# Performance work log

Measured on AMD Instinct MI355X. Metric: run time of the kernel, lower is better.

The kernel has to match this reference:

```python
import jax, jax.numpy as jnp
import numpy as np
from jax import lax
from jax.scipy.special import logsumexp

B, S, H, L = 64, 512, 1024, 9

def setup_inputs() -> dict:
    key = jax.random.key(0)
    ks = jax.random.split(key, 7)
    return {
        'sequence_output': jax.random.normal(ks[0], (B, S, H), dtype=jnp.float32),
        'tags': jax.random.randint(ks[1], (B, S), 0, L, dtype=jnp.int32),
        'mask': jnp.ones((B, S), dtype=bool),
        'W': jax.random.normal(ks[2], (L, H), dtype=jnp.float32) * 0.02,
        'b': jax.random.normal(ks[3], (L,), dtype=jnp.float32) * 0.02,
        'start_transitions': jax.random.normal(ks[4], (L,), dtype=jnp.float32) * 0.1,
        'end_transitions': jax.random.normal(ks[5], (L,), dtype=jnp.float32) * 0.1,
        'transitions': jax.random.normal(ks[6], (L,), dtype=jnp.float32).repeat(1) if False else jax.random.normal(ks[6], (L, L), dtype=jnp.float32) * 0.1,
    }

def _crf_nll(emissions, tags, mask, start_transitions, end_transitions, transitions):
    # emissions: [B,S,L], tags: [B,S] int, mask: [B,S] bool (mask[:,0] all True)
    Bn, Sn, Ln = emissions.shape
    maskf = mask.astype(emissions.dtype)
    bidx = jnp.arange(Bn)
    # ---- numerator: score of the gold tag sequence ----
    score = start_transitions[tags[:, 0]] + emissions[bidx, 0, tags[:, 0]]
    trans_sc = transitions[tags[:, :-1], tags[:, 1:]]                      # [B,S-1]
    emit_sc = jnp.take_along_axis(emissions, tags[..., None].astype(jnp.int32), axis=2)[..., 0]  # [B,S]
    score = score + jnp.sum((trans_sc + emit_sc[:, 1:]) * maskf[:, 1:], axis=1)
    seq_ends = jnp.sum(mask.astype(jnp.int32), axis=1) - 1                 # [B]
    last_tags = tags[bidx, seq_ends]
    score = score + end_transitions[last_tags]
    # ---- denominator: log partition via forward algorithm (scan over time) ----
    em_t = jnp.swapaxes(emissions, 0, 1)   # [S,B,L]
    mk_t = jnp.swapaxes(mask, 0, 1)        # [S,B]
    alpha0 = start_transitions + em_t[0]   # [B,L]
    def step(alpha, xs):
        em, m = xs
        nxt = logsumexp(alpha[:, :, None] + transitions[None] + em[:, None, :], axis=1)
        alpha = jnp.where(m[:, None], nxt, alpha)
        return alpha, None
    alpha, _ = lax.scan(step, alpha0, (em_t[1:], mk_t[1:]))
    logZ = logsumexp(alpha + end_transitions, axis=1)  # [B]
    llh = jnp.sum(score - logZ)  # reduction='sum'
    return -llh

def reference(sequence_output, tags, mask, W, b, start_transitions, end_transitions, transitions):
    # dropout is identity in eval/reference mode
    emissions = jnp.einsum('bsh,lh->bsl', sequence_output, W) + b
    return _crf_nll(emissions, tags, mask, start_transitions, end_transitions, transitions)
```

## Files before the change

### kernel.cpp

```cpp
#include <hip/hip_runtime.h>
#include <math.h>

#define Bn 64
#define Sn 512
#define Hn 1024
#define Ln 9
#define NC 32
#define KC 16
#define NROWS (Bn * Sn)

__global__ __launch_bounds__(256, 2) void emis_kernel(
    const float* __restrict__ seq, const float* __restrict__ W,
    const float* __restrict__ bias, float* __restrict__ em) {
  const int lane = threadIdx.x & 63;
  const int wave = (int)((blockIdx.x * blockDim.x + threadIdx.x) >> 6);
  const int nwave = (int)((gridDim.x * blockDim.x) >> 6);

  float4 w[Ln][4];
#pragma unroll
  for (int l = 0; l < Ln; ++l)
#pragma unroll
    for (int c = 0; c < 4; ++c)
      w[l][c] = *(const float4*)(W + l * Hn + c * 256 + lane * 4);

  float bl[Ln];
#pragma unroll
  for (int l = 0; l < Ln; ++l) bl[l] = bias[l];

  int row = wave;
  float4 x[4];
  if (row < NROWS) {
    const float* p = seq + (size_t)row * Hn;
#pragma unroll
    for (int c = 0; c < 4; ++c) x[c] = *(const float4*)(p + c * 256 + lane * 4);
  }

  for (; row < NROWS; row += nwave) {
    const int nrow = row + nwave;
    float4 xn[4];
    if (nrow < NROWS) {
      const float* p2 = seq + (size_t)nrow * Hn;
#pragma unroll
      for (int c = 0; c < 4; ++c)
        xn[c] = *(const float4*)(p2 + c * 256 + lane * 4);
    }

    float acc[Ln];
#pragma unroll
    for (int l = 0; l < Ln; ++l) {
      float a = x[0].x * w[l][0].x + x[0].y * w[l][0].y +
                x[0].z * w[l][0].z + x[0].w * w[l][0].w;
#pragma unroll
      for (int c = 1; c < 4; ++c) {
        a += x[c].x * w[l][c].x;
        a += x[c].y * w[l][c].y;
        a += x[c].z * w[l][c].z;
        a += x[c].w * w[l][c].w;
      }
      acc[l] = a;
    }
#pragma unroll
    for (int l = 0; l < Ln; ++l) {
      float v = acc[l];
#pragma unroll
      for (int off = 32; off > 0; off >>= 1) v += __shfl_xor(v, off);
      acc[l] = v;
    }
    if (lane < Ln) {
      float v = acc[0] + bl[0];
#pragma unroll
      for (int l = 1; l < Ln; ++l)
        if (lane == l) v = acc[l] + bl[l];
      em[(size_t)row * Ln + lane] = v;
    }
#pragma unroll
    for (int c = 0; c < 4; ++c) x[c] = xn[c];
  }
}

__global__ __launch_bounds__(128) void crf_chunk_kernel(
    const float* __restrict__ em, const float* __restrict__ trans,
    float* __restrict__ Mout) {
  const int bc = blockIdx.x;
  const int b = bc >> 5, c = bc & (NC - 1);
  const int tid = threadIdx.x;
  __shared__ float Mlds[2][Ln][12];
  __shared__ float emlds[KC * Ln];

  const int t0 = c * KC;
  for (int idx = tid; idx < KC * Ln; idx += 128)
    emlds[idx] = em[((size_t)b * Sn + t0) * Ln + idx];

  const bool act = (tid < 81);
  const int i = tid / 9, j = tid - i * 9;
  float Treg[Ln];
  if (act) {
#pragma unroll
    for (int k = 0; k < Ln; ++k) Treg[k] = trans[k * Ln + j];
  }

  const int tb = (c == 0) ? 1 : t0;
  float val = 0.f;
  if (act) {
    val = trans[i * Ln + j] + emlds[(tb - t0) * Ln + j];
    Mlds[0][i][j] = val;
  }
  __syncthreads();

  int cur = 0;
  for (int t = tb + 1; t < t0 + KC; ++t) {
    if (act) {
      float Mr[Ln];
#pragma unroll
      for (int k = 0; k < Ln; ++k) Mr[k] = Mlds[cur][i][k];
      float e = emlds[(t - t0) * Ln + j];
      float m = Mr[0];
#pragma unroll
      for (int k = 1; k < Ln; ++k) m = fmaxf(m, Mr[k]);
      float s = 0.f;
#pragma unroll
      for (int k = 0; k < Ln; ++k) s += __expf(Mr[k] - m + Treg[k]);
      val = m + __logf(s) + e;
      Mlds[cur ^ 1][i][j] = val;
    }
    __syncthreads();
    cur ^= 1;
  }
  if (act) Mout[(size_t)bc * 81 + tid] = val;
}

__global__ __launch_bounds__(64) void crf_combine_kernel(
    const float* __restrict__ em, const int* __restrict__ tags,
    const float* __restrict__ trans, const float* __restrict__ startT,
    const float* __restrict__ endT, const float* __restrict__ Mall,
    float* __restrict__ out) {
  const int b = blockIdx.x;
  const int lane = threadIdx.x;
  const float* emb = em + (size_t)b * Sn * Ln;
  const int* tg = tags + b * Sn;

  float sc = 0.f;
  for (int t = lane; t < Sn; t += 64) {
    int cur = tg[t];
    if (t == 0) {
      sc += startT[cur] + emb[cur];
    } else {
      int prev = tg[t - 1];
      sc += trans[prev * Ln + cur] + emb[t * Ln + cur];
    }
  }
#pragma unroll
  for (int off = 32; off > 0; off >>= 1) sc += __shfl_xor(sc, off);

  const int j = (lane < Ln) ? lane : 0;
  const float* Mb = Mall + (size_t)b * NC * 81;

  float alpha[Ln];
#pragma unroll
  for (int i = 0; i < Ln; ++i) alpha[i] = startT[i] + emb[i];

  float col[Ln];
#pragma unroll
  for (int i = 0; i < Ln; ++i) col[i] = Mb[i * 9 + j];

  for (int cc = 0; cc < NC; ++cc) {
    float ncol[Ln];
    if (cc + 1 < NC) {
#pragma unroll
      for (int i = 0; i < Ln; ++i) ncol[i] = Mb[(cc + 1) * 81 + i * 9 + j];
    }
    float m = alpha[0];
#pragma unroll
    for (int i = 1; i < Ln; ++i) m = fmaxf(m, alpha[i]);
    float s = 0.f;
#pragma unroll
    for (int i = 0; i < Ln; ++i) s += __expf(alpha[i] - m + col[i]);
    float nxt = m + __logf(s);
#pragma unroll
    for (int i = 0; i < Ln; ++i) alpha[i] = __shfl(nxt, i);
#pragma unroll
    for (int i = 0; i < Ln; ++i) col[i] = ncol[i];
  }

  float mf = alpha[0] + endT[0];
#pragma unroll
  for (int i = 1; i < Ln; ++i) mf = fmaxf(mf, alpha[i] + endT[i]);
  float z = 0.f;
#pragma unroll
  for (int i = 0; i < Ln; ++i) z += __expf(alpha[i] + endT[i] - mf);
  float logZ = mf + __logf(z);

  if (lane == 0) {
    float score = sc + endT[tg[Sn - 1]];
    atomicAdd(out, logZ - score);
  }
}

extern "C" void kernel_launch(void* const* d_in, const int* in_sizes, int n_in,
                              void* d_out, int out_size, void* d_ws, size_t ws_size,
                              hipStream_t stream) {
  const float* seq    = (const float*)d_in[0];
  const int*   tags   = (const int*)d_in[1];
  const float* W      = (const float*)d_in[3];
  const float* bias   = (const float*)d_in[4];
  const float* startT = (const float*)d_in[5];
  const float* endT   = (const float*)d_in[6];
  const float* trans  = (const float*)d_in[7];

  float* em   = (float*)d_ws;
  float* Mall = (float*)((char*)d_ws + (size_t)Bn * Sn * Ln * 4);

  hipMemsetAsync(d_out, 0, sizeof(float), stream);
  emis_kernel<<<1024, 256, 0, stream>>>(seq, W, bias, em);
  crf_chunk_kernel<<<Bn * NC, 128, 0, stream>>>(em, trans, Mall);
  crf_combine_kernel<<<Bn, 64, 0, stream>>>(em, tags, trans, startT, endT, Mall,
                                            (float*)d_out);
}
```

Baseline: 236.7 us.

## Fuse emission GEMV with per-chunk CRF transfer matrices and gold-path scoring

The emission projection and the chunked forward-algorithm kernel are merged into one kernel. Each block computes the 16 emission rows for its chunk into LDS, then builds the chunk's 9x9 log-space transfer matrix from them, so emissions never round-trip through global memory. The gold-path score is now computed per chunk with an atomic, and chunk 0 runs the alpha recursion directly. The combine kernel only folds the remaining chunks. In exchange, each block reloads W into registers and only 4 waves stream 16 rows each, which may expose more load latency than the old persistent grid-stride loop.

```diff
diff --git a/kernel.cpp b/kernel.cpp
--- a/kernel.cpp
+++ b/kernel.cpp
@@ -7,42 +7,49 @@
 #define Ln 9
 #define NC 32
 #define KC 16
-#define NROWS (Bn * Sn)
-
-__global__ __launch_bounds__(256, 2) void emis_kernel(
-    const float* __restrict__ seq, const float* __restrict__ W,
-    const float* __restrict__ bias, float* __restrict__ em) {
-  const int lane = threadIdx.x & 63;
-  const int wave = (int)((blockIdx.x * blockDim.x + threadIdx.x) >> 6);
-  const int nwave = (int)((gridDim.x * blockDim.x) >> 6);
+
+__global__ __launch_bounds__(256, 2) void crf_fused(
+    const float* __restrict__ seq, const int* __restrict__ tags,
+    const float* __restrict__ W, const float* __restrict__ bias,
+    const float* __restrict__ startT, const float* __restrict__ endT,
+    const float* __restrict__ trans, float* __restrict__ Mall,
+    float* __restrict__ alphaBuf, float* __restrict__ out) {
+  const int bc = blockIdx.x;
+  const int b = bc >> 5, c = bc & (NC - 1);
+  const int tid = threadIdx.x;
+  const int lane = tid & 63;
+  const int wv = tid >> 6;
+
+  __shared__ float em_lds[KC][Ln];
+  __shared__ float Mlds[2][Ln][12];
+
+  const int t0 = c * KC;
 
   float4 w[Ln][4];
 #pragma unroll
   for (int l = 0; l < Ln; ++l)
 #pragma unroll
-    for (int c = 0; c < 4; ++c)
-      w[l][c] = *(const float4*)(W + l * Hn + c * 256 + lane * 4);
+    for (int c4 = 0; c4 < 4; ++c4)
+      w[l][c4] = *(const float4*)(W + l * Hn + c4 * 256 + lane * 4);
 
   float bl[Ln];
 #pragma unroll
   for (int l = 0; l < Ln; ++l) bl[l] = bias[l];
 
-  int row = wave;
+  const float* rowbase = seq + ((size_t)b * Sn + t0 + wv * 4) * Hn;
   float4 x[4];
-  if (row < NROWS) {
-    const float* p = seq + (size_t)row * Hn;
-#pragma unroll
-    for (int c = 0; c < 4; ++c) x[c] = *(const float4*)(p + c * 256 + lane * 4);
-  }
-
-  for (; row < NROWS; row += nwave) {
-    const int nrow = row + nwave;
+#pragma unroll
+  for (int c4 = 0; c4 < 4; ++c4)
+    x[c4] = *(const float4*)(rowbase + c4 * 256 + lane * 4);
+
+#pragma unroll
+  for (int r = 0; r < 4; ++r) {
     float4 xn[4];
-    if (nrow < NROWS) {
-      const float* p2 = seq + (size_t)nrow * Hn;
-#pragma unroll
-      for (int c = 0; c < 4; ++c)
-        xn[c] = *(const float4*)(p2 + c * 256 + lane * 4);
+    if (r < 3) {
+      const float* p2 = rowbase + (size_t)(r + 1) * Hn;
+#pragma unroll
+      for (int c4 = 0; c4 < 4; ++c4)
+        xn[c4] = *(const float4*)(p2 + c4 * 256 + lane * 4);
     }
 
     float acc[Ln];
@@ -51,11 +58,11 @@
       float a = x[0].x * w[l][0].x + x[0].y * w[l][0].y +
                 x[0].z * w[l][0].z + x[0].w * w[l][0].w;
 #pragma unroll
-      for (int c = 1; c < 4; ++c) {
-        a += x[c].x * w[l][c].x;
-        a += x[c].y * w[l][c].y;
-        a += x[c].z * w[l][c].z;
-        a += x[c].w * w[l][c].w;
+      for (int c4 = 1; c4 < 4; ++c4) {
+        a += x[c4].x * w[l][c4].x;
+        a += x[c4].y * w[l][c4].y;
+        a += x[c4].z * w[l][c4].z;
+        a += x[c4].w * w[l][c4].w;
       }
       acc[l] = a;
     }
@@ -71,99 +78,110 @@
 #pragma unroll
       for (int l = 1; l < Ln; ++l)
         if (lane == l) v = acc[l] + bl[l];
-      em[(size_t)row * Ln + lane] = v;
-    }
-#pragma unroll
-    for (int c = 0; c < 4; ++c) x[c] = xn[c];
+      em_lds[wv * 4 + r][lane] = v;
+    }
+#pragma unroll
+    for (int c4 = 0; c4 < 4; ++c4) x[c4] = xn[c4];
+  }
+  __syncthreads();
+
+  if (wv == 0) {
+    float g = 0.f;
+    if (lane < KC) {
+      const int t = t0 + lane;
+      const int cur = tags[b * Sn + t];
+      const float e = em_lds[lane][cur];
+      if (t == 0) {
+        g = startT[cur] + e;
+      } else {
+        const int prev = tags[b * Sn + t - 1];
+        g = trans[prev * Ln + cur] + e;
+      }
+      if (t == Sn - 1) g += endT[cur];
+    }
+#pragma unroll
+    for (int off = 8; off > 0; off >>= 1) g += __shfl_xor(g, off);
+    if (lane == 0) atomicAdd(out, -g);
+  }
+
+  if (c == 0) {
+    if (wv == 0) {
+      const int j = (lane < Ln) ? lane : 0;
+      float Tcol[Ln];
+#pragma unroll
+      for (int i = 0; i < Ln; ++i) Tcol[i] = trans[i * Ln + j];
+      float alpha[Ln];
+#pragma unroll
+      for (int i = 0; i < Ln; ++i) alpha[i] = startT[i] + em_lds[0][i];
+
+      for (int t = 1; t < KC; ++t) {
+        float m = alpha[0];
+#pragma unroll
+        for (int i = 1; i < Ln; ++i) m = fmaxf(m, alpha[i]);
+        float s = 0.f;
+#pragma unroll
+        for (int i = 0; i < Ln; ++i) s += __expf(alpha[i] - m + Tcol[i]);
+        float nxt = m + __logf(s) + em_lds[t][j];
+#pragma unroll
+        for (int i = 0; i < Ln; ++i) alpha[i] = __shfl(nxt, i);
+      }
+      if (lane < Ln) alphaBuf[b * 16 + lane] = alpha[lane];
+    }
+  } else {
+    const bool act = (tid < 81);
+    const int i = tid / 9, j = tid - i * 9;
+    float Treg[Ln];
+    if (act) {
+#pragma unroll
+      for (int k = 0; k < Ln; ++k) Treg[k] = trans[k * Ln + j];
+    }
+    float val = 0.f;
+    if (act) {
+      val = trans[i * Ln + j] + em_lds[0][j];
+      Mlds[0][i][j] = val;
+    }
+    __syncthreads();
+
+    int cur = 0;
+    for (int t = 1; t < KC; ++t) {
+      if (act) {
+        float Mr[Ln];
+#pragma unroll
+        for (int k = 0; k < Ln; ++k) Mr[k] = Mlds[cur][i][k];
+        float e = em_lds[t][j];
+        float m = Mr[0];
+#pragma unroll
+        for (int k = 1; k < Ln; ++k) m = fmaxf(m, Mr[k]);
+        float s = 0.f;
+#pragma unroll
+        for (int k = 0; k < Ln; ++k) s += __expf(Mr[k] - m + Treg[k]);
+        val = m + __logf(s) + e;
+        Mlds[cur ^ 1][i][j] = val;
+      }
+      __syncthreads();
+      cur ^= 1;
+    }
+    if (act) Mall[(size_t)bc * 81 + tid] = val;
   }
 }
 
-__global__ __launch_bounds__(128) void crf_chunk_kernel(
-    const float* __restrict__ em, const float* __restrict__ trans,
-    float* __restrict__ Mout) {
-  const int bc = blockIdx.x;
-  const int b = bc >> 5, c = bc & (NC - 1);
-  const int tid = threadIdx.x;
-  __shared__ float Mlds[2][Ln][12];
-  __shared__ float emlds[KC * Ln];
-
-  const int t0 = c * KC;
-  for (int idx = tid; idx < KC * Ln; idx += 128)
-    emlds[idx] = em[((size_t)b * Sn + t0) * Ln + idx];
-
-  const bool act = (tid < 81);
-  const int i = tid / 9, j = tid - i * 9;
-  float Treg[Ln];
-  if (act) {
-#pragma unroll
-    for (int k = 0; k < Ln; ++k) Treg[k] = trans[k * Ln + j];
-  }
-
-  const int tb = (c == 0) ? 1 : t0;
-  float val = 0.f;
-  if (act) {
-    val = trans[i * Ln + j] + emlds[(tb - t0) * Ln + j];
-    Mlds[0][i][j] = val;
-  }
-  __syncthreads();
-
-  int cur = 0;
-  for (int t = tb + 1; t < t0 + KC; ++t) {
-    if (act) {
-      float Mr[Ln];
-#pragma unroll
-      for (int k = 0; k < Ln; ++k) Mr[k] = Mlds[cur][i][k];
-      float e = emlds[(t - t0) * Ln + j];
-      float m = Mr[0];
-#pragma unroll
-      for (int k = 1; k < Ln; ++k) m = fmaxf(m, Mr[k]);
-      float s = 0.f;
-#pragma unroll
-      for (int k = 0; k < Ln; ++k) s += __expf(Mr[k] - m + Treg[k]);
-      val = m + __logf(s) + e;
-      Mlds[cur ^ 1][i][j] = val;
-    }
-    __syncthreads();
-    cur ^= 1;
-  }
-  if (act) Mout[(size_t)bc * 81 + tid] = val;
-}
-
-__global__ __launch_bounds__(64) void crf_combine_kernel(
-    const float* __restrict__ em, const int* __restrict__ tags,
-    const float* __restrict__ trans, const float* __restrict__ startT,
-    const float* __restrict__ endT, const float* __restrict__ Mall,
-    float* __restrict__ out) {
+__global__ __launch_bounds__(64) void crf_combine(
+    const float* __restrict__ Mall, const float* __restrict__ alphaBuf,
+    const float* __restrict__ endT, float* __restrict__ out) {
   const int b = blockIdx.x;
   const int lane = threadIdx.x;
-  const float* emb = em + (size_t)b * Sn * Ln;
-  const int* tg = tags + b * Sn;
-
-  float sc = 0.f;
-  for (int t = lane; t < Sn; t += 64) {
-    int cur = tg[t];
-    if (t == 0) {
-      sc += startT[cur] + emb[cur];
-    } else {
-      int prev = tg[t - 1];
-      sc += trans[prev * Ln + cur] + emb[t * Ln + cur];
-    }
-  }
-#pragma unroll
-  for (int off = 32; off > 0; off >>= 1) sc += __shfl_xor(sc, off);
-
   const int j = (lane < Ln) ? lane : 0;
   const float* Mb = Mall + (size_t)b * NC * 81;
 
   float alpha[Ln];
 #pragma unroll
-  for (int i = 0; i < Ln; ++i) alpha[i] = startT[i] + emb[i];
+  for (int i = 0; i < Ln; ++i) alpha[i] = alphaBuf[b * 16 + i];
 
   float col[Ln];
 #pragma unroll
-  for (int i = 0; i < Ln; ++i) col[i] = Mb[i * 9 + j];
-
-  for (int cc = 0; cc < NC; ++cc) {
+  for (int i = 0; i < Ln; ++i) col[i] = Mb[81 + i * 9 + j];
+
+  for (int cc = 1; cc < NC; ++cc) {
     float ncol[Ln];
     if (cc + 1 < NC) {
 #pragma unroll
@@ -190,10 +208,7 @@
   for (int i = 0; i < Ln; ++i) z += __expf(alpha[i] + endT[i] - mf);
   float logZ = mf + __logf(z);
 
-  if (lane == 0) {
-    float score = sc + endT[tg[Sn - 1]];
-    atomicAdd(out, logZ - score);
-  }
+  if (lane == 0) atomicAdd(out, logZ);
 }
 
 extern "C" void kernel_launch(void* const* d_in, const int* in_sizes, int n_in,
@@ -207,12 +222,11 @@
   const float* endT   = (const float*)d_in[6];
   const float* trans  = (const float*)d_in[7];
 
-  float* em   = (float*)d_ws;
-  float* Mall = (float*)((char*)d_ws + (size_t)Bn * Sn * Ln * 4);
+  float* Mall     = (float*)d_ws;
+  float* alphaBuf = Mall + (size_t)Bn * NC * 81;
 
   hipMemsetAsync(d_out, 0, sizeof(float), stream);
-  emis_kernel<<<1024, 256, 0, stream>>>(seq, W, bias, em);
-  crf_chunk_kernel<<<Bn * NC, 128, 0, stream>>>(em, trans, Mall);
-  crf_combine_kernel<<<Bn, 64, 0, stream>>>(em, tags, trans, startT, endT, Mall,
-                                            (float*)d_out);
+  crf_fused<<<Bn * NC, 256, 0, stream>>>(seq, tags, W, bias, startT, endT,
+                                         trans, Mall, alphaBuf, (float*)d_out);
+  crf_combine<<<Bn, 64, 0, stream>>>(Mall, alphaBuf, endT, (float*)d_out);
 }
```

New measurement: 232.5 us. No clear change (-1.8%).
